# Performance work log

Measured on AMD Instinct MI355X. Metric: run time of the kernel, lower is better.

The kernel has to match this reference:

```python
import jax, jax.numpy as jnp
import numpy as np
from jax import lax

DIM = 256; HEADS = 16; DHEAD = 16; H = 12; W = 26
DS = 4; KOFF = 6; OSCALE = 4.0
SCALE = DHEAD ** -0.5
EPS = 1e-5


def _create_grid(hh, ww, dtype):
    # channel0 = x (width index), channel1 = y (height index); matches torch meshgrid(arange(w), arange(h), indexing='xy')
    gy, gx = jnp.meshgrid(jnp.arange(hh, dtype=dtype), jnp.arange(ww, dtype=dtype), indexing='ij')
    return jnp.stack([gx, gy], axis=0)  # (2, hh, ww)


def _grid_sample_bilinear(img, grid):
    # F.grid_sample, mode='bilinear', padding_mode='zeros', align_corners=False
    # img (B,C,Hi,Wi); grid (B,Ho,Wo,2), grid[...,0]=x-norm, grid[...,1]=y-norm in [-1,1]
    B, C, Hi, Wi = img.shape
    x = ((grid[..., 0] + 1.0) * Wi - 1.0) / 2.0
    y = ((grid[..., 1] + 1.0) * Hi - 1.0) / 2.0
    x0 = jnp.floor(x); y0 = jnp.floor(y)

    def gather(xi, yi):
        valid = ((xi >= 0) & (xi < Wi) & (yi >= 0) & (yi < Hi)).astype(img.dtype)
        xc = jnp.clip(xi, 0, Wi - 1).astype(jnp.int32)
        yc = jnp.clip(yi, 0, Hi - 1).astype(jnp.int32)
        v = jax.vmap(lambda im, yy, xx: im[:, yy, xx])(img, yc, xc)  # (B,C,Ho,Wo)
        return v * valid[:, None]

    wx1 = (x - x0)[:, None]; wx0 = 1.0 - wx1
    wy1 = (y - y0)[:, None]; wy0 = 1.0 - wy1
    return (gather(x0, y0) * wy0 * wx0 + gather(x0 + 1.0, y0) * wy0 * wx1
            + gather(x0, y0 + 1.0) * wy1 * wx0 + gather(x0 + 1.0, y0 + 1.0) * wy1 * wx1)


def _forward(x, q, w_off_dw, b_off_dw, w_off_pw, wk, wv, w_out, b_out,
             cpb_w1, cpb_b1, cpb_w2, cpb_b2, cpb_w3, cpb_b3,
             conv1d_w, conv1d_b, ln_g, ln_b):
    b = x.shape[0]
    # faithful to torch: q.repeat(1,1,h*w).view(bs,1,dim,h,w).squeeze(1) == tile then reshape
    q_map = jnp.tile(q[:, 0, :], (1, H * W)).reshape(b, DIM, H, W)

    # to_offsets: depthwise Conv2d(k=6,s=4,p=1) -> GELU -> 1x1 conv (no bias) -> tanh -> *offset_scale
    t = lax.conv_general_dilated(q_map, w_off_dw, window_strides=(DS, DS),
                                 padding=[(1, 1), (1, 1)], feature_group_count=DIM,
                                 dimension_numbers=('NCHW', 'OIHW', 'NCHW'))
    t = jax.nn.gelu(t + b_off_dw[None, :, None, None], approximate=False)
    off = jnp.tanh(jnp.einsum('oc,bchw->bohw', w_off_pw, t)) * OSCALE  # (b,2,Hk,Wk)
    Hk, Wk = off.shape[-2], off.shape[-1]  # 3, 6

    gkv = _create_grid(Hk, Wk, x.dtype)
    vg0 = gkv[0] + off[:, 0]
    vg1 = gkv[1] + off[:, 1]
    # faithful repo normalize_grid: channel0 / (h-1), channel1 / (w-1)
    n0 = 2.0 * vg0 / max(Hk - 1, 1) - 1.0
    n1 = 2.0 * vg1 / max(Wk - 1, 1) - 1.0
    vgrid_scaled = jnp.stack([n0, n1], axis=-1)  # (b, Hk, Wk, 2)

    kv = _grid_sample_bilinear(x, vgrid_scaled)  # (b, DIM, Hk, Wk)
    k = jnp.einsum('oc,bchw->bohw', wk, kv)
    v = jnp.einsum('oc,bchw->bohw', wv, kv)

    qh = (q_map * SCALE).reshape(b, HEADS, DHEAD, H * W).transpose(0, 1, 3, 2)  # (b,h,i,d)
    kh = k.reshape(b, HEADS, DHEAD, Hk * Wk).transpose(0, 1, 3, 2)              # (b,h,j,d)
    vh = v.reshape(b, HEADS, DHEAD, Hk * Wk).transpose(0, 1, 3, 2)
    sim = jnp.einsum('bhid,bhjd->bhij', qh, kh)  # (b,16,312,18)

    # CPB relative position bias
    gq = _create_grid(H, W, x.dtype)
    gq0 = 2.0 * gq[0] / max(H - 1, 1) - 1.0
    gq1 = 2.0 * gq[1] / max(W - 1, 1) - 1.0
    grid_q = jnp.stack([gq0, gq1], axis=-1).reshape(1, H * W, 2)
    grid_kv = vgrid_scaled.reshape(b, Hk * Wk, 2)
    pos = grid_q[:, :, None, :] - grid_kv[:, None, :, :]       # (b,i,j,2)
    bias = jnp.sign(pos) * jnp.log(jnp.abs(pos) + 1.0)
    bias = jax.nn.relu(bias @ cpb_w1.T + cpb_b1)
    bias = jax.nn.relu(bias @ cpb_w2.T + cpb_b2)
    bias = bias @ cpb_w3.T + cpb_b3                             # (b,i,j,heads)
    sim = sim + bias.transpose(0, 3, 1, 2)

    attn = jax.nn.softmax(sim, axis=-1)  # dropout(0.1) identity in eval
    out = jnp.einsum('bhij,bhjd->bhid', attn, vh)               # (b,h,i,d)
    out = out.transpose(0, 1, 3, 2).reshape(b, DIM, H, W)        # 'b h (x y) d -> b (h d) x y'
    out = jnp.einsum('oc,bchw->bohw', w_out, out) + b_out[None, :, None, None]

    # SpatialCrossAttention tail: view -> permute -> Conv1d(312,1,1) -> residual -> LayerNorm
    tokens = out.reshape(b, DIM, H * W).transpose(0, 2, 1)       # (b,312,256)
    pooled = jnp.einsum('t,btc->bc', conv1d_w, tokens)[:, None, :] + conv1d_b[None, :, None]
    y = pooled + q
    mu = y.mean(-1, keepdims=True)
    var = y.var(-1, keepdims=True)
    return (y - mu) / jnp.sqrt(var + EPS) * ln_g + ln_b          # (b,1,256)


def setup_inputs() -> dict:
    key = jax.random.key(0)
    ks = jax.random.split(key, 16)
    rn = lambda i, shape, s=0.02: jax.random.normal(ks[i], shape, dtype=jnp.float32) * s
    B = 256
    return {
        'x': jax.random.normal(ks[0], (B, DIM, H, W), dtype=jnp.float32),
        'q': jax.random.normal(ks[1], (B, 1, DIM), dtype=jnp.float32),
        'w_off_dw': rn(2, (DIM, 1, KOFF, KOFF), 0.05),
        'b_off_dw': jnp.zeros((DIM,), jnp.float32),
        'w_off_pw': rn(3, (2, DIM), 0.05),
        'wk': rn(4, (DIM, DIM)),
        'wv': rn(5, (DIM, DIM)),
        'w_out': rn(6, (DIM, DIM)),
        'b_out': jnp.zeros((DIM,), jnp.float32),
        'cpb_w1': rn(7, (64, 2), 0.1),
        'cpb_b1': jnp.zeros((64,), jnp.float32),
        'cpb_w2': rn(8, (64, 64), 0.1),
        'cpb_b2': jnp.zeros((64,), jnp.float32),
        'cpb_w3': rn(9, (HEADS, 64), 0.1),
        'cpb_b3': jnp.zeros((HEADS,), jnp.float32),
        'conv1d_w': rn(10, (H * W,), 0.05),
        'conv1d_b': jnp.zeros((1,), jnp.float32),
        'ln_g': jnp.ones((DIM,), jnp.float32),
        'ln_b': jnp.zeros((DIM,), jnp.float32),
    }


def reference(x, q, w_off_dw, b_off_dw, w_off_pw, wk, wv, w_out, b_out,
              cpb_w1, cpb_b1, cpb_w2, cpb_b2, cpb_w3, cpb_b3,
              conv1d_w, conv1d_b, ln_g, ln_b):
    return _forward(x, q, w_off_dw, b_off_dw, w_off_pw, wk, wv, w_out, b_out,
                    cpb_w1, cpb_b1, cpb_w2, cpb_b2, cpb_w3, cpb_b3,
                    conv1d_w, conv1d_b, ln_g, ln_b)
```

## Files before the change

### kernel.cpp

```cpp
#include <hip/hip_runtime.h>
#include <math.h>


typedef __attribute__((ext_vector_type(8))) short short8;
typedef __attribute__((ext_vector_type(4))) float floatx4;

union U16 { uint4 u; short8 s; };

__device__ __forceinline__ unsigned int f2bf(float f) {
    unsigned int u = __float_as_uint(f);
    u += 0x7fffu + ((u >> 16) & 1u);
    return u >> 16;
}
__device__ __forceinline__ unsigned int pk2(float a, float b) {
    return f2bf(a) | (f2bf(b) << 16);
}
__device__ __forceinline__ float bf2f(unsigned short v) {
    return __uint_as_float((unsigned int)v << 16);
}

#define WSF_W2 16384
#define WSF_W3 16896
#define WSF_DW 68096

__global__ __launch_bounds__(256) void k0_setup(
    const float* __restrict__ wk, const float* __restrict__ wv,
    const float* __restrict__ cw2, const float* __restrict__ cw3,
    const float* __restrict__ w_dw, unsigned int* __restrict__ ws)
{
    const int t = blockIdx.x * 256 + threadIdx.x;
    uint4* ws4 = (uint4*)ws;
    {
        const int m2 = t >> 13;
        const int r = t & 8191;
        const int mt = r >> 9, ks = (r >> 6) & 7, lane = r & 63;
        const int nn = lane & 15, qd = lane >> 4;
        const float* src = (m2 ? wv : wk) + (mt * 16 + nn) * 256 + ks * 32 + qd * 8;
        uint4 o;
        o.x = pk2(src[0], src[1]); o.y = pk2(src[2], src[3]);
        o.z = pk2(src[4], src[5]); o.w = pk2(src[6], src[7]);
        ws4[t] = o;
    }
    if (t < 512) {
        const int mt = t >> 7, ks = (t >> 6) & 1, lane = t & 63;
        const int nn = lane & 15, qd = lane >> 4;
        const float* src = cw2 + (mt * 16 + nn) * 64 + ks * 32 + qd * 8;
        uint4 o;
        o.x = pk2(src[0], src[1]); o.y = pk2(src[2], src[3]);
        o.z = pk2(src[4], src[5]); o.w = pk2(src[6], src[7]);
        ws4[WSF_W2 + t] = o;
    }
    if (t < 128) {
        const int ks = t >> 6, lane = t & 63;
        const int nn = lane & 15, qd = lane >> 4;
        const float* src = cw3 + nn * 64 + ks * 32 + qd * 8;
        uint4 o;
        o.x = pk2(src[0], src[1]); o.y = pk2(src[2], src[3]);
        o.z = pk2(src[4], src[5]); o.w = pk2(src[6], src[7]);
        ws4[WSF_W3 + t] = o;
    }
    float* wsf = (float*)ws;
    for (int k = t; k < 9216; k += 16384) {
        const int c = k / 36, i = k - c * 36;
        wsf[WSF_DW + i * 256 + c] = w_dw[k];
    }
}

__global__ __launch_bounds__(512, 2) void k_fused(
    const float* __restrict__ x, const float* __restrict__ q,
    const float* __restrict__ b_dw, const float* __restrict__ w_pw,
    const float* __restrict__ cw1, const float* __restrict__ cb1,
    const float* __restrict__ cb2, const float* __restrict__ cb3,
    const float* __restrict__ conv_w, const float* __restrict__ conv_b,
    const float* __restrict__ w_out, const float* __restrict__ b_out,
    const float* __restrict__ ln_g, const float* __restrict__ ln_b,
    const unsigned int* __restrict__ ws, float* __restrict__ out)
{
    const int b = blockIdx.x, tid = threadIdx.x;
    const int w = tid >> 6, lane = tid & 63;
    const int n = lane & 15, qd = lane >> 4;

    __shared__ float qf_s[256];
    __shared__ unsigned short q_sb[256];
    __shared__ unsigned short v_sb[5120];
    __shared__ float F0[468], F1[216];
    __shared__ unsigned int lutxy[312];
    __shared__ float off_s[36], n0_s[18], n1_s[18];
    __shared__ float sx0[18], sy0[18], swx[18], swy[18];
    __shared__ float wA_s[288];
    __shared__ __align__(16) float m_s[256];
    __shared__ float pooled_s[256], redb[16];
    __shared__ __align__(16) unsigned char UB[38464];
    float* S_ = (float*)UB;
    unsigned short* kvT = (unsigned short*)UB;
    float* qsw = (float*)UB;
    float* t_s = (float*)(UB + 16512);
    unsigned short* k_sb = (unsigned short*)(UB + 20000);
    unsigned int* h2w = (unsigned int*)(UB + 20000);

    const uint4* ws4 = (const uint4*)ws;
    const float* wsf = (const float*)ws;

    uint4 W2f[4][2], W3f[2];
    #pragma unroll
    for (int mtl = 0; mtl < 4; ++mtl)
        #pragma unroll
        for (int ks = 0; ks < 2; ++ks)
            W2f[mtl][ks] = ws4[WSF_W2 + mtl * 128 + ks * 64 + lane];
    W3f[0] = ws4[WSF_W3 + lane];
    W3f[1] = ws4[WSF_W3 + 64 + lane];

    float W1a[16], W1b[16], B1r[16];
    #pragma unroll
    for (int kk = 0; kk < 16; ++kk) {
        const int kid = (kk < 8) ? (qd * 8 + kk) : (32 + qd * 8 + kk - 8);
        W1a[kk] = cw1[kid * 2]; W1b[kk] = cw1[kid * 2 + 1]; B1r[kk] = cb1[kid];
    }
    float bb2[16];
    #pragma unroll
    for (int mtl = 0; mtl < 4; ++mtl)
        #pragma unroll
        for (int r = 0; r < 4; ++r) bb2[mtl * 4 + r] = cb2[mtl * 16 + qd * 4 + r];
    float bb3[4];
    #pragma unroll
    for (int r = 0; r < 4; ++r) bb3[r] = cb3[qd * 4 + r];

    if (tid < 256) {
        const float qv = q[b * 256 + tid];
        qf_s[tid] = qv;
        q_sb[tid] = (unsigned short)f2bf(qv * 0.25f);
    }
    for (int u = tid; u < 4128; u += 512) {
        const int r = u / 258, i = u - r * 258;
        qsw[u] = (i < 256) ? q[b * 256 + i] : 0.f;
    }
    for (int u = tid; u < 312; u += 512) {
        const int iy = u / 26;
        lutxy[u] = (unsigned int)(u - iy * 26) | ((unsigned int)iy << 16);
    }
    __syncthreads();

    {
        const int c = tid & 255, g = tid >> 8;
        float wreg[36];
        #pragma unroll
        for (int i = 0; i < 36; ++i) wreg[i] = wsf[WSF_DW + i * 256 + c];
        float acc[9];
        const float bv = b_dw[c];
        #pragma unroll
        for (int a = 0; a < 9; ++a) acc[a] = bv;
        const int cb = (c * 56) & 255;
        const int cp = (c & 15) * 258;
        for (int jh = 0; jh < 3; ++jh) {
            for (int kh = 0; kh < 6; ++kh) {
                const int ih = jh * 4 - 1 + kh;
                if (ih < 0 || ih >= 12) continue;
                const int rb = ih * 26;
                #pragma unroll
                for (int jwl = 0; jwl < 3; ++jwl) {
                    const int jw = g * 3 + jwl;
                    #pragma unroll
                    for (int kw = 0; kw < 6; ++kw) {
                        const int iw = jw * 4 - 1 + kw;
                        if (iw < 0 || iw >= 26) continue;
                        acc[jh * 3 + jwl] += wreg[kh * 6 + kw] * qsw[cp + ((cb + rb + iw) & 255)];
                    }
                }
            }
        }
        #pragma unroll
        for (int a = 0; a < 9; ++a) {
            const int jh = a / 3, jwl = a - jh * 3;
            const int p = jh * 6 + g * 3 + jwl;
            const float v = acc[a];
            t_s[p * 256 + c] = 0.5f * v * (1.0f + erff(v * 0.70710678118654752f));
        }
    }
    __syncthreads();

    for (int oi = w; oi < 36; oi += 8) {
        const int o = oi / 18, p = oi - o * 18;
        float s = 0.f;
        for (int c = lane; c < 256; c += 64) s += w_pw[o * 256 + c] * t_s[p * 256 + c];
        for (int d = 32; d > 0; d >>= 1) s += __shfl_down(s, d, 64);
        if (lane == 0) off_s[oi] = 4.0f * tanhf(s);
    }
    __syncthreads();

    if (tid < 18) {
        const int j = tid, jh = j / 6, jw = j - jh * 6;
        const float vg0 = (float)jw + off_s[j];
        const float vg1 = (float)jh + off_s[18 + j];
        const float n0 = 2.0f * vg0 / 2.0f - 1.0f;
        const float n1 = 2.0f * vg1 / 5.0f - 1.0f;
        n0_s[j] = n0; n1_s[j] = n1;
        const float xp = ((n0 + 1.0f) * 26.0f - 1.0f) * 0.5f;
        const float yp = ((n1 + 1.0f) * 12.0f - 1.0f) * 0.5f;
        const float x0 = floorf(xp), y0 = floorf(yp);
        sx0[j] = x0; sy0[j] = y0; swx[j] = xp - x0; swy[j] = yp - y0;
    }
    __syncthreads();

    {
        const int c = tid & 255, g = tid >> 8;
        const float* xb = x + ((size_t)b * 256 + c) * 312;
        for (int jj = 0; jj < 9; ++jj) {
            const int j = g * 9 + jj;
            const int x0 = (int)sx0[j], y0 = (int)sy0[j];
            const int x1 = x0 + 1, y1 = y0 + 1;
            const float wx1 = swx[j], wy1 = swy[j];
            const float wx0 = 1.f - wx1, wy0 = 1.f - wy1;
            const bool xv0 = (x0 >= 0) & (x0 < 26), xv1 = (x1 >= 0) & (x1 < 26);
            const bool yv0 = (y0 >= 0) & (y0 < 12), yv1 = (y1 >= 0) & (y1 < 12);
            const float v00 = (xv0 & yv0) ? xb[y0 * 26 + x0] : 0.f;
            const float v01 = (xv1 & yv0) ? xb[y0 * 26 + x1] : 0.f;
            const float v10 = (xv0 & yv1) ? xb[y1 * 26 + x0] : 0.f;
            const float v11 = (xv1 & yv1) ? xb[y1 * 26 + x1] : 0.f;
            const float val = wy0 * (wx0 * v00 + wx1 * v01) + wy1 * (wx0 * v10 + wx1 * v11);
            kvT[j * 264 + c] = (unsigned short)f2bf(val);
        }
    }
    for (int u = tid; u < 684; u += 512) {
        if (u < 468) {
            const int ixv = u / 18, j = u - ixv * 18;
            const float p0 = (float)ixv * (2.0f / 11.0f) - 1.0f - n0_s[j];
            F0[u] = copysignf(__logf(1.0f + fabsf(p0)), p0);
        } else {
            const int u2 = u - 468;
            const int iyv = u2 / 18, j = u2 - iyv * 18;
            const float p1 = (float)iyv * (2.0f / 25.0f) - 1.0f - n1_s[j];
            F1[u2] = copysignf(__logf(1.0f + fabsf(p1)), p1);
        }
    }
    __syncthreads();

    {
        const int m2 = w & 1, mtb = w >> 1;
        floatx4 pa[4][2];
        #pragma unroll
        for (int a = 0; a < 4; ++a) {
            pa[a][0] = (floatx4){0.f, 0.f, 0.f, 0.f};
            pa[a][1] = (floatx4){0.f, 0.f, 0.f, 0.f};
        }
        for (int ks = 0; ks < 8; ++ks) {
            U16 b0, b1;
            b0.u = *(const uint4*)(kvT + n * 264 + ks * 32 + qd * 8);
            b1.u = make_uint4(0u, 0u, 0u, 0u);
            if (n < 2) b1.u = *(const uint4*)(kvT + (16 + n) * 264 + ks * 32 + qd * 8);
            #pragma unroll
            for (int mtl = 0; mtl < 4; ++mtl) {
                const int mt = mtb + mtl * 4;
                U16 A; A.u = ws4[m2 * 8192 + mt * 512 + ks * 64 + lane];
                pa[mtl][0] = __builtin_amdgcn_mfma_f32_16x16x32_bf16(A.s, b0.s, pa[mtl][0], 0, 0, 0);
                pa[mtl][1] = __builtin_amdgcn_mfma_f32_16x16x32_bf16(A.s, b1.s, pa[mtl][1], 0, 0, 0);
            }
        }
        unsigned short* dst = m2 ? v_sb : k_sb;
        #pragma unroll
        for (int mtl = 0; mtl < 4; ++mtl) {
            const int mt = mtb + mtl * 4;
            #pragma unroll
            for (int r = 0; r < 4; ++r) {
                const int o = mt * 16 + qd * 4 + r;
                dst[o * 20 + n] = (unsigned short)f2bf(pa[mtl][0][r]);
                if (n < 2) dst[o * 20 + 16 + n] = (unsigned short)f2bf(pa[mtl][1][r]);
            }
        }
    }
    __syncthreads();

    uint4 BkU[2][2];
    #pragma unroll
    for (int hh = 0; hh < 2; ++hh)
        #pragma unroll
        for (int jt = 0; jt < 2; ++jt) {
            unsigned int u0 = 0, u1 = 0, u2 = 0, u3 = 0;
            if (qd < 2 && (jt == 0 || n < 2)) {
                const int h = w * 2 + hh;
                const int j = jt * 16 + n;
                const int cb0 = (h * 16 + qd * 8) * 20 + j;
                u0 = (unsigned)k_sb[cb0] | ((unsigned)k_sb[cb0 + 20] << 16);
                u1 = (unsigned)k_sb[cb0 + 40] | ((unsigned)k_sb[cb0 + 60] << 16);
                u2 = (unsigned)k_sb[cb0 + 80] | ((unsigned)k_sb[cb0 + 100] << 16);
                u3 = (unsigned)k_sb[cb0 + 120] | ((unsigned)k_sb[cb0 + 140] << 16);
            }
            BkU[hh][jt] = make_uint4(u0, u1, u2, u3);
        }
    __syncthreads();

    float wAcc[18];
    #pragma unroll
    for (int j = 0; j < 18; ++j) wAcc[j] = 0.f;

    for (int ch = 0; ch < 20; ++ch) {
        const int ibase = ch * 16;
        const int CI = (ch == 19) ? 8 : 16;

        #pragma unroll
        for (int hh = 0; hh < 2; ++hh) {
            const int h = w * 2 + hh;
            unsigned int a0 = 0, a1 = 0, a2 = 0, a3u = 0;
            if (qd < 2) {
                const int base = h * 16 + qd * 8;
                a0 = (unsigned)q_sb[((base + 0) * 56 + ibase + n) & 255] |
                     ((unsigned)q_sb[((base + 1) * 56 + ibase + n) & 255] << 16);
                a1 = (unsigned)q_sb[((base + 2) * 56 + ibase + n) & 255] |
                     ((unsigned)q_sb[((base + 3) * 56 + ibase + n) & 255] << 16);
                a2 = (unsigned)q_sb[((base + 4) * 56 + ibase + n) & 255] |
                     ((unsigned)q_sb[((base + 5) * 56 + ibase + n) & 255] << 16);
                a3u = (unsigned)q_sb[((base + 6) * 56 + ibase + n) & 255] |
                      ((unsigned)q_sb[((base + 7) * 56 + ibase + n) & 255] << 16);
            }
            U16 Af; Af.u = make_uint4(a0, a1, a2, a3u);
            #pragma unroll
            for (int jt = 0; jt < 2; ++jt) {
                U16 Bf; Bf.u = BkU[hh][jt];
                floatx4 D = {0.f, 0.f, 0.f, 0.f};
                D = __builtin_amdgcn_mfma_f32_16x16x32_bf16(Af.s, Bf.s, D, 0, 0, 0);
                const int j = jt * 16 + n;
                if (j < 18) {
                    #pragma unroll
                    for (int r = 0; r < 4; ++r)
                        S_[((qd * 4 + r) * 18 + j) * 17 + h] = D[r];
                }
            }
        }
        __syncthreads();

        {
            const int i0 = ibase + n;
            const unsigned int lv = lutxy[i0 < 312 ? i0 : 311];
            const int ix = (int)(lv & 0xffffu), iy = (int)(lv >> 16);
            for (int nt = w; nt < 18; nt += 8) {
                const float f0 = F0[ix * 18 + nt];
                const float f1 = F1[iy * 18 + nt];
                float h1v[16];
                #pragma unroll
                for (int kk = 0; kk < 16; ++kk)
                    h1v[kk] = fmaxf(fmaf(W1a[kk], f0, fmaf(W1b[kk], f1, B1r[kk])), 0.f);
                U16 ub0, ub1;
                ub0.u = make_uint4(pk2(h1v[0], h1v[1]), pk2(h1v[2], h1v[3]),
                                   pk2(h1v[4], h1v[5]), pk2(h1v[6], h1v[7]));
                ub1.u = make_uint4(pk2(h1v[8], h1v[9]), pk2(h1v[10], h1v[11]),
                                   pk2(h1v[12], h1v[13]), pk2(h1v[14], h1v[15]));
                floatx4 g2[4];
                #pragma unroll
                for (int mtl = 0; mtl < 4; ++mtl) {
                    U16 A0; A0.u = W2f[mtl][0];
                    U16 A1; A1.u = W2f[mtl][1];
                    floatx4 acc = {0.f, 0.f, 0.f, 0.f};
                    acc = __builtin_amdgcn_mfma_f32_16x16x32_bf16(A0.s, ub0.s, acc, 0, 0, 0);
                    acc = __builtin_amdgcn_mfma_f32_16x16x32_bf16(A1.s, ub1.s, acc, 0, 0, 0);
                    g2[mtl] = acc;
                }
                unsigned int* hw = h2w + w * 576 + n * 36;
                #pragma unroll
                for (int mtl = 0; mtl < 4; ++mtl) {
                    const float e0 = fmaxf(g2[mtl][0] + bb2[mtl * 4 + 0], 0.f);
                    const float e1 = fmaxf(g2[mtl][1] + bb2[mtl * 4 + 1], 0.f);
                    const float e2 = fmaxf(g2[mtl][2] + bb2[mtl * 4 + 2], 0.f);
                    const float e3 = fmaxf(g2[mtl][3] + bb2[mtl * 4 + 3], 0.f);
                    hw[mtl * 8 + qd * 2]     = pk2(e0, e1);
                    hw[mtl * 8 + qd * 2 + 1] = pk2(e2, e3);
                }
                U16 uc0, uc1;
                uc0.u = *(const uint4*)(hw + qd * 4);
                uc1.u = *(const uint4*)(hw + 16 + qd * 4);
                floatx4 a3 = {0.f, 0.f, 0.f, 0.f};
                {
                    U16 A0; A0.u = W3f[0]; U16 A1; A1.u = W3f[1];
                    a3 = __builtin_amdgcn_mfma_f32_16x16x32_bf16(A0.s, uc0.s, a3, 0, 0, 0);
                    a3 = __builtin_amdgcn_mfma_f32_16x16x32_bf16(A1.s, uc1.s, a3, 0, 0, 0);
                }
                float* sp = S_ + (n * 18 + nt) * 17 + qd * 4;
                #pragma unroll
                for (int r = 0; r < 4; ++r) sp[r] = a3[r] + bb3[r] + sp[r];
            }
        }
        __syncthreads();

        if (tid < 256) {
            const int il = tid >> 4, h = tid & 15;
            if (il < CI) {
                float lv[18];
                #pragma unroll
                for (int j = 0; j < 18; ++j) lv[j] = S_[(il * 18 + j) * 17 + h];
                float m = lv[0];
                #pragma unroll
                for (int j = 1; j < 18; ++j) m = fmaxf(m, lv[j]);
                float s = 0.f;
                #pragma unroll
                for (int j = 0; j < 18; ++j) { lv[j] = __expf(lv[j] - m); s += lv[j]; }
                const float wgt = conv_w[ibase + il] / s;
                #pragma unroll
                for (int j = 0; j < 18; ++j) wAcc[j] = fmaf(wgt, lv[j], wAcc[j]);
            }
        }
        __syncthreads();
    }

    if (tid < 256) {
        const int il = tid >> 4, h = tid & 15;
        float* wred = (float*)UB;
        #pragma unroll
        for (int j = 0; j < 18; ++j) wred[(il * 16 + h) * 18 + j] = wAcc[j];
    }
    __syncthreads();
    {
        const float* wred = (const float*)UB;
        for (int u = tid; u < 288; u += 512) {
            const int h = u / 18, j = u - h * 18;
            float s = 0.f;
            #pragma unroll
            for (int il = 0; il < 16; ++il) s += wred[(il * 16 + h) * 18 + j];
            wA_s[u] = s;
        }
    }
    {
        float v = 0.f;
        for (int u = tid; u < 312; u += 512) v += conv_w[u];
        for (int d = 32; d > 0; d >>= 1) v += __shfl_down(v, d, 64);
        if (lane == 0) redb[w] = v;
    }
    __syncthreads();

    if (tid < 256) {
        const int c = tid;
        const int hb = (c >> 4) * 18;
        float acc = 0.f;
        #pragma unroll
        for (int j = 0; j < 18; ++j) acc += wA_s[hb + j] * bf2f(v_sb[c * 20 + j]);
        m_s[c] = acc;
    }
    __syncthreads();

    const float Ssum = redb[0] + redb[1] + redb[2] + redb[3] +
                       redb[4] + redb[5] + redb[6] + redb[7];

    {
        const float4 mm = *(const float4*)(m_s + lane * 4);
        for (int ol = 0; ol < 32; ++ol) {
            const int o = w * 32 + ol;
            const float4 wq = *(const float4*)(w_out + o * 256 + lane * 4);
            float d = wq.x * mm.x + wq.y * mm.y + wq.z * mm.z + wq.w * mm.w;
            for (int dd = 32; dd > 0; dd >>= 1) d += __shfl_down(d, dd, 64);
            if (lane == 0) pooled_s[o] = d;
        }
    }
    __syncthreads();

    if (tid < 256) {
        const int o = tid;
        const float y = pooled_s[o] + b_out[o] * Ssum + conv_b[0] + qf_s[o];
        float s1 = y, s2 = y * y;
        for (int d = 32; d > 0; d >>= 1) { s1 += __shfl_down(s1, d, 64); s2 += __shfl_down(s2, d, 64); }
        if (lane == 0) { redb[8 + w] = s1; redb[12 + w] = s2; }
    }
    __syncthreads();
    if (tid < 256) {
        const int o = tid;
        const float y = pooled_s[o] + b_out[o] * Ssum + conv_b[0] + qf_s[o];
        const float S1 = redb[8] + redb[9] + redb[10] + redb[11];
        const float S2 = redb[12] + redb[13] + redb[14] + redb[15];
        const float mu = S1 * (1.0f / 256.0f);
        const float var = S2 * (1.0f / 256.0f) - mu * mu;
        out[b * 256 + o] = (y - mu) * rsqrtf(var + 1e-5f) * ln_g[o] + ln_b[o];
    }
}

extern "C" void kernel_launch(void* const* d_in, const int* in_sizes, int n_in,
                              void* d_out, int out_size, void* d_ws, size_t ws_size,
                              hipStream_t stream) {
    const float* x       = (const float*)d_in[0];
    const float* q       = (const float*)d_in[1];
    const float* w_dw    = (const float*)d_in[2];
    const float* b_dwp   = (const float*)d_in[3];
    const float* w_pw    = (const float*)d_in[4];
    const float* wk      = (const float*)d_in[5];
    const float* wv      = (const float*)d_in[6];
    const float* w_out   = (const float*)d_in[7];
    const float* b_out   = (const float*)d_in[8];
    const float* cw1     = (const float*)d_in[9];
    const float* cb1     = (const float*)d_in[10];
    const float* cw2     = (const float*)d_in[11];
    const float* cb2     = (const float*)d_in[12];
    const float* cw3     = (const float*)d_in[13];
    const float* cb3     = (const float*)d_in[14];
    const float* conv_w  = (const float*)d_in[15];
    const float* conv_b  = (const float*)d_in[16];
    const float* ln_g    = (const float*)d_in[17];
    const float* ln_b    = (const float*)d_in[18];
    float* out = (float*)d_out;
    unsigned int* ws = (unsigned int*)d_ws;

    k0_setup<<<64, 256, 0, stream>>>(wk, wv, cw2, cw3, w_dw, ws);
    k_fused<<<256, 512, 0, stream>>>(x, q, b_dwp, w_pw, cw1, cb1, cb2, cb3,
                                     conv_w, conv_b, w_out, b_out, ln_g, ln_b,
                                     (const unsigned int*)ws, out);
}
```

Baseline: 268.1 us.

## Double fused kernel block to 1024 threads and redistribute work per wave

The fused kernel moves from 512 to 1024 threads per block. Every phase is re-partitioned for 16 waves: each wave owns one head instead of two, chunks cover 32 query positions instead of 16, and the shared-memory buffers grow to match. The CPB weight fragments now load into registers later, and the bias vectors move from registers to LDS, to relieve register pressure under the tighter launch bounds. With one block of 256 per batch element the aim is more latency hiding and fewer chunk iterations, at the cost of more LDS, larger barriers and possible register spills under __launch_bounds__(1024,4).

```diff
diff --git a/kernel.cpp b/kernel.cpp
--- a/kernel.cpp
+++ b/kernel.cpp
@@ -66,7 +66,7 @@
     }
 }
 
-__global__ __launch_bounds__(512, 2) void k_fused(
+__global__ __launch_bounds__(1024, 4) void k_fused(
     const float* __restrict__ x, const float* __restrict__ q,
     const float* __restrict__ b_dw, const float* __restrict__ w_pw,
     const float* __restrict__ cw1, const float* __restrict__ cb1,
@@ -79,6 +79,7 @@
     const int b = blockIdx.x, tid = threadIdx.x;
     const int w = tid >> 6, lane = tid & 63;
     const int n = lane & 15, qd = lane >> 4;
+    const int c = tid & 255, g = tid >> 8;
 
     __shared__ float qf_s[256];
     __shared__ unsigned short q_sb[256];
@@ -87,101 +88,67 @@
     __shared__ unsigned int lutxy[312];
     __shared__ float off_s[36], n0_s[18], n1_s[18];
     __shared__ float sx0[18], sy0[18], swx[18], swy[18];
-    __shared__ float wA_s[288];
+    __shared__ float wA_s[288], b2_s[64], b3_s[16];
     __shared__ __align__(16) float m_s[256];
-    __shared__ float pooled_s[256], redb[16];
-    __shared__ __align__(16) unsigned char UB[38464];
+    __shared__ float pooled_s[256], redb[24];
+    __shared__ __align__(16) unsigned char UB[89344];
     float* S_ = (float*)UB;
     unsigned short* kvT = (unsigned short*)UB;
     float* qsw = (float*)UB;
     float* t_s = (float*)(UB + 16512);
-    unsigned short* k_sb = (unsigned short*)(UB + 20000);
-    unsigned int* h2w = (unsigned int*)(UB + 20000);
+    unsigned short* k_sb = (unsigned short*)(UB + 16512);
+    unsigned int* h2w = (unsigned int*)(UB + 48384);
+    float* wred = (float*)UB;
 
     const uint4* ws4 = (const uint4*)ws;
     const float* wsf = (const float*)ws;
-
-    uint4 W2f[4][2], W3f[2];
-    #pragma unroll
-    for (int mtl = 0; mtl < 4; ++mtl)
-        #pragma unroll
-        for (int ks = 0; ks < 2; ++ks)
-            W2f[mtl][ks] = ws4[WSF_W2 + mtl * 128 + ks * 64 + lane];
-    W3f[0] = ws4[WSF_W3 + lane];
-    W3f[1] = ws4[WSF_W3 + 64 + lane];
-
-    float W1a[16], W1b[16], B1r[16];
-    #pragma unroll
-    for (int kk = 0; kk < 16; ++kk) {
-        const int kid = (kk < 8) ? (qd * 8 + kk) : (32 + qd * 8 + kk - 8);
-        W1a[kk] = cw1[kid * 2]; W1b[kk] = cw1[kid * 2 + 1]; B1r[kk] = cb1[kid];
-    }
-    float bb2[16];
-    #pragma unroll
-    for (int mtl = 0; mtl < 4; ++mtl)
-        #pragma unroll
-        for (int r = 0; r < 4; ++r) bb2[mtl * 4 + r] = cb2[mtl * 16 + qd * 4 + r];
-    float bb3[4];
-    #pragma unroll
-    for (int r = 0; r < 4; ++r) bb3[r] = cb3[qd * 4 + r];
 
     if (tid < 256) {
         const float qv = q[b * 256 + tid];
         qf_s[tid] = qv;
         q_sb[tid] = (unsigned short)f2bf(qv * 0.25f);
     }
-    for (int u = tid; u < 4128; u += 512) {
+    for (int u = tid; u < 4128; u += 1024) {
         const int r = u / 258, i = u - r * 258;
         qsw[u] = (i < 256) ? q[b * 256 + i] : 0.f;
     }
-    for (int u = tid; u < 312; u += 512) {
-        const int iy = u / 26;
-        lutxy[u] = (unsigned int)(u - iy * 26) | ((unsigned int)iy << 16);
-    }
-    __syncthreads();
-
-    {
-        const int c = tid & 255, g = tid >> 8;
+    if (tid < 312) {
+        const int iy = tid / 26;
+        lutxy[tid] = (unsigned int)(tid - iy * 26) | ((unsigned int)iy << 16);
+    }
+    if (tid < 64) b2_s[tid] = cb2[tid];
+    if (tid < 16) b3_s[tid] = cb3[tid];
+    __syncthreads();
+
+    {
         float wreg[36];
         #pragma unroll
         for (int i = 0; i < 36; ++i) wreg[i] = wsf[WSF_DW + i * 256 + c];
-        float acc[9];
         const float bv = b_dw[c];
-        #pragma unroll
-        for (int a = 0; a < 9; ++a) acc[a] = bv;
         const int cb = (c * 56) & 255;
         const int cp = (c & 15) * 258;
-        for (int jh = 0; jh < 3; ++jh) {
+        for (int p = g; p < 18; p += 4) {
+            const int jh = p / 6, jw = p - jh * 6;
+            float acc = bv;
             for (int kh = 0; kh < 6; ++kh) {
                 const int ih = jh * 4 - 1 + kh;
                 if (ih < 0 || ih >= 12) continue;
                 const int rb = ih * 26;
-                #pragma unroll
-                for (int jwl = 0; jwl < 3; ++jwl) {
-                    const int jw = g * 3 + jwl;
-                    #pragma unroll
-                    for (int kw = 0; kw < 6; ++kw) {
-                        const int iw = jw * 4 - 1 + kw;
-                        if (iw < 0 || iw >= 26) continue;
-                        acc[jh * 3 + jwl] += wreg[kh * 6 + kw] * qsw[cp + ((cb + rb + iw) & 255)];
-                    }
+                for (int kw = 0; kw < 6; ++kw) {
+                    const int iw = jw * 4 - 1 + kw;
+                    if (iw < 0 || iw >= 26) continue;
+                    acc += wreg[kh * 6 + kw] * qsw[cp + ((cb + rb + iw) & 255)];
                 }
             }
-        }
-        #pragma unroll
-        for (int a = 0; a < 9; ++a) {
-            const int jh = a / 3, jwl = a - jh * 3;
-            const int p = jh * 6 + g * 3 + jwl;
-            const float v = acc[a];
-            t_s[p * 256 + c] = 0.5f * v * (1.0f + erff(v * 0.70710678118654752f));
-        }
-    }
-    __syncthreads();
-
-    for (int oi = w; oi < 36; oi += 8) {
+            t_s[p * 256 + c] = 0.5f * acc * (1.0f + erff(acc * 0.70710678118654752f));
+        }
+    }
+    __syncthreads();
+
+    for (int oi = w; oi < 36; oi += 16) {
         const int o = oi / 18, p = oi - o * 18;
         float s = 0.f;
-        for (int c = lane; c < 256; c += 64) s += w_pw[o * 256 + c] * t_s[p * 256 + c];
+        for (int cc = lane; cc < 256; cc += 64) s += w_pw[o * 256 + cc] * t_s[p * 256 + cc];
         for (int d = 32; d > 0; d >>= 1) s += __shfl_down(s, d, 64);
         if (lane == 0) off_s[oi] = 4.0f * tanhf(s);
     }
@@ -202,10 +169,8 @@
     __syncthreads();
 
     {
-        const int c = tid & 255, g = tid >> 8;
         const float* xb = x + ((size_t)b * 256 + c) * 312;
-        for (int jj = 0; jj < 9; ++jj) {
-            const int j = g * 9 + jj;
+        for (int j = g; j < 18; j += 4) {
             const int x0 = (int)sx0[j], y0 = (int)sy0[j];
             const int x1 = x0 + 1, y1 = y0 + 1;
             const float wx1 = swx[j], wy1 = swy[j];
@@ -220,13 +185,13 @@
             kvT[j * 264 + c] = (unsigned short)f2bf(val);
         }
     }
-    for (int u = tid; u < 684; u += 512) {
-        if (u < 468) {
-            const int ixv = u / 18, j = u - ixv * 18;
+    if (tid < 684) {
+        if (tid < 468) {
+            const int ixv = tid / 18, j = tid - ixv * 18;
             const float p0 = (float)ixv * (2.0f / 11.0f) - 1.0f - n0_s[j];
-            F0[u] = copysignf(__logf(1.0f + fabsf(p0)), p0);
+            F0[tid] = copysignf(__logf(1.0f + fabsf(p0)), p0);
         } else {
-            const int u2 = u - 468;
+            const int u2 = tid - 468;
             const int iyv = u2 / 18, j = u2 - iyv * 18;
             const float p1 = (float)iyv * (2.0f / 25.0f) - 1.0f - n1_s[j];
             F1[u2] = copysignf(__logf(1.0f + fabsf(p1)), p1);
@@ -236,9 +201,9 @@
 
     {
         const int m2 = w & 1, mtb = w >> 1;
-        floatx4 pa[4][2];
-        #pragma unroll
-        for (int a = 0; a < 4; ++a) {
+        floatx4 pa[2][2];
+        #pragma unroll
+        for (int a = 0; a < 2; ++a) {
             pa[a][0] = (floatx4){0.f, 0.f, 0.f, 0.f};
             pa[a][1] = (floatx4){0.f, 0.f, 0.f, 0.f};
         }
@@ -248,8 +213,8 @@
             b1.u = make_uint4(0u, 0u, 0u, 0u);
             if (n < 2) b1.u = *(const uint4*)(kvT + (16 + n) * 264 + ks * 32 + qd * 8);
             #pragma unroll
-            for (int mtl = 0; mtl < 4; ++mtl) {
-                const int mt = mtb + mtl * 4;
+            for (int mtl = 0; mtl < 2; ++mtl) {
+                const int mt = mtb + mtl * 8;
                 U16 A; A.u = ws4[m2 * 8192 + mt * 512 + ks * 64 + lane];
                 pa[mtl][0] = __builtin_amdgcn_mfma_f32_16x16x32_bf16(A.s, b0.s, pa[mtl][0], 0, 0, 0);
                 pa[mtl][1] = __builtin_amdgcn_mfma_f32_16x16x32_bf16(A.s, b1.s, pa[mtl][1], 0, 0, 0);
@@ -257,8 +222,8 @@
         }
         unsigned short* dst = m2 ? v_sb : k_sb;
         #pragma unroll
-        for (int mtl = 0; mtl < 4; ++mtl) {
-            const int mt = mtb + mtl * 4;
+        for (int mtl = 0; mtl < 2; ++mtl) {
+            const int mt = mtb + mtl * 8;
             #pragma unroll
             for (int r = 0; r < 4; ++r) {
                 const int o = mt * 16 + qd * 4 + r;
@@ -269,122 +234,130 @@
     }
     __syncthreads();
 
-    uint4 BkU[2][2];
+    uint4 BkU[2];
     #pragma unroll
-    for (int hh = 0; hh < 2; ++hh)
-        #pragma unroll
-        for (int jt = 0; jt < 2; ++jt) {
-            unsigned int u0 = 0, u1 = 0, u2 = 0, u3 = 0;
-            if (qd < 2 && (jt == 0 || n < 2)) {
-                const int h = w * 2 + hh;
-                const int j = jt * 16 + n;
-                const int cb0 = (h * 16 + qd * 8) * 20 + j;
-                u0 = (unsigned)k_sb[cb0] | ((unsigned)k_sb[cb0 + 20] << 16);
-                u1 = (unsigned)k_sb[cb0 + 40] | ((unsigned)k_sb[cb0 + 60] << 16);
-                u2 = (unsigned)k_sb[cb0 + 80] | ((unsigned)k_sb[cb0 + 100] << 16);
-                u3 = (unsigned)k_sb[cb0 + 120] | ((unsigned)k_sb[cb0 + 140] << 16);
-            }
-            BkU[hh][jt] = make_uint4(u0, u1, u2, u3);
-        }
-    __syncthreads();
+    for (int jt = 0; jt < 2; ++jt) {
+        unsigned int u0 = 0, u1 = 0, u2 = 0, u3 = 0;
+        if (qd < 2 && (jt == 0 || n < 2)) {
+            const int j = jt * 16 + n;
+            const int cb0 = (w * 16 + qd * 8) * 20 + j;
+            u0 = (unsigned)k_sb[cb0] | ((unsigned)k_sb[cb0 + 20] << 16);
+            u1 = (unsigned)k_sb[cb0 + 40] | ((unsigned)k_sb[cb0 + 60] << 16);
+            u2 = (unsigned)k_sb[cb0 + 80] | ((unsigned)k_sb[cb0 + 100] << 16);
+            u3 = (unsigned)k_sb[cb0 + 120] | ((unsigned)k_sb[cb0 + 140] << 16);
+        }
+        BkU[jt] = make_uint4(u0, u1, u2, u3);
+    }
+    __syncthreads();
+
+    uint4 W2f[4][2], W3f[2];
+    #pragma unroll
+    for (int mtl = 0; mtl < 4; ++mtl)
+        #pragma unroll
+        for (int ks = 0; ks < 2; ++ks)
+            W2f[mtl][ks] = ws4[WSF_W2 + mtl * 128 + ks * 64 + lane];
+    W3f[0] = ws4[WSF_W3 + lane];
+    W3f[1] = ws4[WSF_W3 + 64 + lane];
+
+    float W1a[16], W1b[16], B1r[16];
+    #pragma unroll
+    for (int kk = 0; kk < 16; ++kk) {
+        const int kid = (kk < 8) ? (qd * 8 + kk) : (32 + qd * 8 + kk - 8);
+        W1a[kk] = cw1[kid * 2]; W1b[kk] = cw1[kid * 2 + 1]; B1r[kk] = cb1[kid];
+    }
 
     float wAcc[18];
     #pragma unroll
     for (int j = 0; j < 18; ++j) wAcc[j] = 0.f;
 
-    for (int ch = 0; ch < 20; ++ch) {
-        const int ibase = ch * 16;
-        const int CI = (ch == 19) ? 8 : 16;
-
-        #pragma unroll
-        for (int hh = 0; hh < 2; ++hh) {
-            const int h = w * 2 + hh;
+    for (int ch = 0; ch < 10; ++ch) {
+        const int ibase = ch * 32;
+        const int CI = (ch == 9) ? 24 : 32;
+
+        #pragma unroll
+        for (int ig = 0; ig < 2; ++ig) {
             unsigned int a0 = 0, a1 = 0, a2 = 0, a3u = 0;
             if (qd < 2) {
-                const int base = h * 16 + qd * 8;
-                a0 = (unsigned)q_sb[((base + 0) * 56 + ibase + n) & 255] |
-                     ((unsigned)q_sb[((base + 1) * 56 + ibase + n) & 255] << 16);
-                a1 = (unsigned)q_sb[((base + 2) * 56 + ibase + n) & 255] |
-                     ((unsigned)q_sb[((base + 3) * 56 + ibase + n) & 255] << 16);
-                a2 = (unsigned)q_sb[((base + 4) * 56 + ibase + n) & 255] |
-                     ((unsigned)q_sb[((base + 5) * 56 + ibase + n) & 255] << 16);
-                a3u = (unsigned)q_sb[((base + 6) * 56 + ibase + n) & 255] |
-                      ((unsigned)q_sb[((base + 7) * 56 + ibase + n) & 255] << 16);
+                const int base = w * 16 + qd * 8;
+                const int ii = ibase + ig * 16 + n;
+                a0 = (unsigned)q_sb[((base + 0) * 56 + ii) & 255] |
+                     ((unsigned)q_sb[((base + 1) * 56 + ii) & 255] << 16);
+                a1 = (unsigned)q_sb[((base + 2) * 56 + ii) & 255] |
+                     ((unsigned)q_sb[((base + 3) * 56 + ii) & 255] << 16);
+                a2 = (unsigned)q_sb[((base + 4) * 56 + ii) & 255] |
+                     ((unsigned)q_sb[((base + 5) * 56 + ii) & 255] << 16);
+                a3u = (unsigned)q_sb[((base + 6) * 56 + ii) & 255] |
+                      ((unsigned)q_sb[((base + 7) * 56 + ii) & 255] << 16);
             }
             U16 Af; Af.u = make_uint4(a0, a1, a2, a3u);
             #pragma unroll
             for (int jt = 0; jt < 2; ++jt) {
-                U16 Bf; Bf.u = BkU[hh][jt];
+                U16 Bf; Bf.u = BkU[jt];
                 floatx4 D = {0.f, 0.f, 0.f, 0.f};
                 D = __builtin_amdgcn_mfma_f32_16x16x32_bf16(Af.s, Bf.s, D, 0, 0, 0);
                 const int j = jt * 16 + n;
                 if (j < 18) {
                     #pragma unroll
                     for (int r = 0; r < 4; ++r)
-                        S_[((qd * 4 + r) * 18 + j) * 17 + h] = D[r];
+                        S_[((ig * 16 + qd * 4 + r) * 18 + j) * 21 + w] = D[r];
                 }
             }
         }
         __syncthreads();
 
-        {
-            const int i0 = ibase + n;
-            const unsigned int lv = lutxy[i0 < 312 ? i0 : 311];
+        for (int t = w; t < 36; t += 16) {
+            const int ig = (t >= 18) ? 1 : 0;
+            const int j = t - ig * 18;
+            const int i0r = ibase + ig * 16 + n;
+            const unsigned int lv = lutxy[(i0r < 312) ? i0r : 311];
             const int ix = (int)(lv & 0xffffu), iy = (int)(lv >> 16);
-            for (int nt = w; nt < 18; nt += 8) {
-                const float f0 = F0[ix * 18 + nt];
-                const float f1 = F1[iy * 18 + nt];
-                float h1v[16];
-                #pragma unroll
-                for (int kk = 0; kk < 16; ++kk)
-                    h1v[kk] = fmaxf(fmaf(W1a[kk], f0, fmaf(W1b[kk], f1, B1r[kk])), 0.f);
-                U16 ub0, ub1;
-                ub0.u = make_uint4(pk2(h1v[0], h1v[1]), pk2(h1v[2], h1v[3]),
-                                   pk2(h1v[4], h1v[5]), pk2(h1v[6], h1v[7]));
-                ub1.u = make_uint4(pk2(h1v[8], h1v[9]), pk2(h1v[10], h1v[11]),
-                                   pk2(h1v[12], h1v[13]), pk2(h1v[14], h1v[15]));
-                floatx4 g2[4];
-                #pragma unroll
-                for (int mtl = 0; mtl < 4; ++mtl) {
-                    U16 A0; A0.u = W2f[mtl][0];
-                    U16 A1; A1.u = W2f[mtl][1];
-                    floatx4 acc = {0.f, 0.f, 0.f, 0.f};
-                    acc = __builtin_amdgcn_mfma_f32_16x16x32_bf16(A0.s, ub0.s, acc, 0, 0, 0);
-                    acc = __builtin_amdgcn_mfma_f32_16x16x32_bf16(A1.s, ub1.s, acc, 0, 0, 0);
-                    g2[mtl] = acc;
-                }
-                unsigned int* hw = h2w + w * 576 + n * 36;
-                #pragma unroll
-                for (int mtl = 0; mtl < 4; ++mtl) {
-                    const float e0 = fmaxf(g2[mtl][0] + bb2[mtl * 4 + 0], 0.f);
-                    const float e1 = fmaxf(g2[mtl][1] + bb2[mtl * 4 + 1], 0.f);
-                    const float e2 = fmaxf(g2[mtl][2] + bb2[mtl * 4 + 2], 0.f);
-                    const float e3 = fmaxf(g2[mtl][3] + bb2[mtl * 4 + 3], 0.f);
-                    hw[mtl * 8 + qd * 2]     = pk2(e0, e1);
-                    hw[mtl * 8 + qd * 2 + 1] = pk2(e2, e3);
-                }
-                U16 uc0, uc1;
-                uc0.u = *(const uint4*)(hw + qd * 4);
-                uc1.u = *(const uint4*)(hw + 16 + qd * 4);
-                floatx4 a3 = {0.f, 0.f, 0.f, 0.f};
-                {
-                    U16 A0; A0.u = W3f[0]; U16 A1; A1.u = W3f[1];
-                    a3 = __builtin_amdgcn_mfma_f32_16x16x32_bf16(A0.s, uc0.s, a3, 0, 0, 0);
-                    a3 = __builtin_amdgcn_mfma_f32_16x16x32_bf16(A1.s, uc1.s, a3, 0, 0, 0);
-                }
-                float* sp = S_ + (n * 18 + nt) * 17 + qd * 4;
-                #pragma unroll
-                for (int r = 0; r < 4; ++r) sp[r] = a3[r] + bb3[r] + sp[r];
-            }
+            const float f0 = F0[ix * 18 + j];
+            const float f1 = F1[iy * 18 + j];
+            unsigned int uu[8];
+            #pragma unroll
+            for (int kp = 0; kp < 8; ++kp) {
+                const float ha = fmaxf(fmaf(W1a[2 * kp], f0, fmaf(W1b[2 * kp], f1, B1r[2 * kp])), 0.f);
+                const float hb = fmaxf(fmaf(W1a[2 * kp + 1], f0, fmaf(W1b[2 * kp + 1], f1, B1r[2 * kp + 1])), 0.f);
+                uu[kp] = pk2(ha, hb);
+            }
+            U16 ub0, ub1;
+            ub0.u = make_uint4(uu[0], uu[1], uu[2], uu[3]);
+            ub1.u = make_uint4(uu[4], uu[5], uu[6], uu[7]);
+            unsigned int* hw = h2w + w * 640 + n * 40;
+            #pragma unroll
+            for (int mtl = 0; mtl < 4; ++mtl) {
+                U16 A0, A1; A0.u = W2f[mtl][0]; A1.u = W2f[mtl][1];
+                floatx4 acc = {0.f, 0.f, 0.f, 0.f};
+                acc = __builtin_amdgcn_mfma_f32_16x16x32_bf16(A0.s, ub0.s, acc, 0, 0, 0);
+                acc = __builtin_amdgcn_mfma_f32_16x16x32_bf16(A1.s, ub1.s, acc, 0, 0, 0);
+                const float e0 = fmaxf(acc[0] + b2_s[mtl * 16 + qd * 4 + 0], 0.f);
+                const float e1 = fmaxf(acc[1] + b2_s[mtl * 16 + qd * 4 + 1], 0.f);
+                const float e2 = fmaxf(acc[2] + b2_s[mtl * 16 + qd * 4 + 2], 0.f);
+                const float e3 = fmaxf(acc[3] + b2_s[mtl * 16 + qd * 4 + 3], 0.f);
+                hw[mtl * 8 + qd * 2]     = pk2(e0, e1);
+                hw[mtl * 8 + qd * 2 + 1] = pk2(e2, e3);
+            }
+            U16 uc0, uc1;
+            uc0.u = *(const uint4*)(hw + qd * 4);
+            uc1.u = *(const uint4*)(hw + 16 + qd * 4);
+            floatx4 a3 = {0.f, 0.f, 0.f, 0.f};
+            {
+                U16 A0, A1; A0.u = W3f[0]; A1.u = W3f[1];
+                a3 = __builtin_amdgcn_mfma_f32_16x16x32_bf16(A0.s, uc0.s, a3, 0, 0, 0);
+                a3 = __builtin_amdgcn_mfma_f32_16x16x32_bf16(A1.s, uc1.s, a3, 0, 0, 0);
+            }
+            float* sp = S_ + ((ig * 16 + n) * 18 + j) * 21 + qd * 4;
+            #pragma unroll
+            for (int r = 0; r < 4; ++r) sp[r] = a3[r] + b3_s[qd * 4 + r] + sp[r];
         }
         __syncthreads();
 
-        if (tid < 256) {
+        if (tid < 512) {
             const int il = tid >> 4, h = tid & 15;
             if (il < CI) {
                 float lv[18];
                 #pragma unroll
-                for (int j = 0; j < 18; ++j) lv[j] = S_[(il * 18 + j) * 17 + h];
+                for (int j = 0; j < 18; ++j) lv[j] = S_[(il * 18 + j) * 21 + h];
                 float m = lv[0];
                 #pragma unroll
                 for (int j = 1; j < 18; ++j) m = fmaxf(m, lv[j]);
@@ -399,48 +372,44 @@
         __syncthreads();
     }
 
-    if (tid < 256) {
-        const int il = tid >> 4, h = tid & 15;
-        float* wred = (float*)UB;
-        #pragma unroll
-        for (int j = 0; j < 18; ++j) wred[(il * 16 + h) * 18 + j] = wAcc[j];
-    }
-    __syncthreads();
-    {
-        const float* wred = (const float*)UB;
-        for (int u = tid; u < 288; u += 512) {
-            const int h = u / 18, j = u - h * 18;
-            float s = 0.f;
-            #pragma unroll
-            for (int il = 0; il < 16; ++il) s += wred[(il * 16 + h) * 18 + j];
-            wA_s[u] = s;
-        }
+    if (tid < 512) {
+        const int slot = tid >> 4, h = tid & 15;
+        #pragma unroll
+        for (int j = 0; j < 18; ++j) wred[(slot * 16 + h) * 18 + j] = wAcc[j];
     }
     {
         float v = 0.f;
-        for (int u = tid; u < 312; u += 512) v += conv_w[u];
+        for (int u = tid; u < 312; u += 1024) v += conv_w[u];
         for (int d = 32; d > 0; d >>= 1) v += __shfl_down(v, d, 64);
         if (lane == 0) redb[w] = v;
     }
     __syncthreads();
+    for (int u = tid; u < 288; u += 1024) {
+        const int h = u / 18, j = u - h * 18;
+        float s = 0.f;
+        #pragma unroll
+        for (int sl = 0; sl < 32; ++sl) s += wred[(sl * 16 + h) * 18 + j];
+        wA_s[u] = s;
+    }
+    __syncthreads();
 
     if (tid < 256) {
-        const int c = tid;
-        const int hb = (c >> 4) * 18;
+        const int hb = (tid >> 4) * 18;
         float acc = 0.f;
         #pragma unroll
-        for (int j = 0; j < 18; ++j) acc += wA_s[hb + j] * bf2f(v_sb[c * 20 + j]);
-        m_s[c] = acc;
-    }
-    __syncthreads();
-
-    const float Ssum = redb[0] + redb[1] + redb[2] + redb[3] +
-                       redb[4] + redb[5] + redb[6] + redb[7];
+        for (int j = 0; j < 18; ++j) acc += wA_s[hb + j] * bf2f(v_sb[tid * 20 + j]);
+        m_s[tid] = acc;
+    }
+    __syncthreads();
+
+    float Ssum = 0.f;
+    #pragma unroll
+    for (int i = 0; i < 16; ++i) Ssum += redb[i];
 
     {
         const float4 mm = *(const float4*)(m_s + lane * 4);
-        for (int ol = 0; ol < 32; ++ol) {
-            const int o = w * 32 + ol;
+        for (int ol = 0; ol < 16; ++ol) {
+            const int o = w * 16 + ol;
             const float4 wq = *(const float4*)(w_out + o * 256 + lane * 4);
             float d = wq.x * mm.x + wq.y * mm.y + wq.z * mm.z + wq.w * mm.w;
             for (int dd = 32; dd > 0; dd >>= 1) d += __shfl_down(d, dd, 64);
@@ -450,21 +419,19 @@
     __syncthreads();
 
     if (tid < 256) {
-        const int o = tid;
-        const float y = pooled_s[o] + b_out[o] * Ssum + conv_b[0] + qf_s[o];
+        const float y = pooled_s[tid] + b_out[tid] * Ssum + conv_b[0] + qf_s[tid];
         float s1 = y, s2 = y * y;
         for (int d = 32; d > 0; d >>= 1) { s1 += __shfl_down(s1, d, 64); s2 += __shfl_down(s2, d, 64); }
-        if (lane == 0) { redb[8 + w] = s1; redb[12 + w] = s2; }
+        if (lane == 0) { redb[16 + w] = s1; redb[20 + w] = s2; }
     }
     __syncthreads();
     if (tid < 256) {
-        const int o = tid;
-        const float y = pooled_s[o] + b_out[o] * Ssum + conv_b[0] + qf_s[o];
-        const float S1 = redb[8] + redb[9] + redb[10] + redb[11];
-        const float S2 = redb[12] + redb[13] + redb[14] + redb[15];
+        const float y = pooled_s[tid] + b_out[tid] * Ssum + conv_b[0] + qf_s[tid];
+        const float S1 = redb[16] + redb[17] + redb[18] + redb[19];
+        const float S2 = redb[20] + redb[21] + redb[22] + redb[23];
         const float mu = S1 * (1.0f / 256.0f);
         const float var = S2 * (1.0f / 256.0f) - mu * mu;
-        out[b * 256 + o] = (y - mu) * rsqrtf(var + 1e-5f) * ln_g[o] + ln_b[o];
+        out[b * 256 + tid] = (y - mu) * rsqrtf(var + 1e-5f) * ln_g[tid] + ln_b[tid];
     }
 }
 
@@ -494,7 +461,7 @@
     unsigned int* ws = (unsigned int*)d_ws;
 
     k0_setup<<<64, 256, 0, stream>>>(wk, wv, cw2, cw3, w_dw, ws);
-    k_fused<<<256, 512, 0, stream>>>(x, q, b_dwp, w_pw, cw1, cb1, cb2, cb3,
-                                     conv_w, conv_b, w_out, b_out, ln_g, ln_b,
-                                     (const unsigned int*)ws, out);
-}
+    k_fused<<<256, 1024, 0, stream>>>(x, q, b_dwp, w_pw, cw1, cb1, cb2, cb3,
+                                      conv_w, conv_b, w_out, b_out, ln_g, ln_b,
+                                      (const unsigned int*)ws, out);
+}
```

Result: slower. 458.6 us (+71.1%).
